# Kernel tuning notes

Measured on AMD Instinct MI355X. Metric: run time of the kernel, lower is better.

The kernel has to match this reference:

```python
import jax, jax.numpy as jnp
import numpy as np

SEGMENT_LENGTHS = [2048, 4096]
DILATION_RATES = [1, 2]


def _group_attention(qg, kg, vg, seg_len, r, gidx):
    # qg/kg/vg: [b, gh, n, d]; segmented dilated attention for one head group.
    b, gh, n, d = qg.shape
    nseg = n // seg_len
    scale = float(1.0 / np.sqrt(d))
    qs = qg.reshape(b, gh, nseg, seg_len, d)
    ks = kg.reshape(b, gh, nseg, seg_len, d)
    vs = vg.reshape(b, gh, nseg, seg_len, d)
    if r > 1:
        m = seg_len // r
        # offset = (group_idx + seg_idx) % r; pattern = offset + r*arange(m) (no wrap since seg_len % r == 0)
        offsets = (gidx + jnp.arange(nseg)) % r            # [nseg]
        idx = offsets[:, None] + r * jnp.arange(m)[None, :]  # [nseg, m]
        si = jnp.arange(nseg)[:, None]                      # [nseg, 1]
        qd = qs[:, :, si, idx]                              # [b, gh, nseg, m, d]
        kd = ks[:, :, si, idx]
        vd = vs[:, :, si, idx]
    else:
        qd, kd, vd = qs, ks, vs
    scores = jnp.einsum('bgsqd,bgskd->bgsqk', qd, kd) * scale
    attn = jax.nn.softmax(scores, axis=-1)
    out = jnp.einsum('bgsqk,bgskd->bgsqd', attn, vd)
    if r > 1:
        # scatter dilated outputs back to their segment positions; unselected positions stay 0
        full = jnp.zeros((b, gh, nseg, seg_len, d), dtype=qg.dtype)
        out = full.at[:, :, si, idx].set(out)
    return out.reshape(b, gh, n, d)


def reference(q, k, v):
    # q, k, v: [b, n, h, d]; ring_size == 1 -> single-device dilated attention
    b, n, h, d = q.shape
    ngroups = len(SEGMENT_LENGTHS)
    gsize = h // ngroups
    qt = jnp.transpose(q, (0, 2, 1, 3))  # [b, h, n, d]
    kt = jnp.transpose(k, (0, 2, 1, 3))
    vt = jnp.transpose(v, (0, 2, 1, 3))
    outs = []
    for i, (s, r) in enumerate(zip(SEGMENT_LENGTHS, DILATION_RATES)):
        hs, he = i * gsize, (i + 1) * gsize
        outs.append(_group_attention(qt[:, hs:he], kt[:, hs:he], vt[:, hs:he], s, r, i))
    out = jnp.concatenate(outs, axis=1)   # [b, h, n, d]
    return jnp.transpose(out, (0, 2, 1, 3))  # [b, n, h, d]


def setup_inputs() -> dict:
    key = jax.random.key(0)
    kq, kk, kv = jax.random.split(key, 3)
    shape = (1, 8192, 16, 128)
    return {
        'q': jax.random.normal(kq, shape, dtype=jnp.float32),
        'k': jax.random.normal(kk, shape, dtype=jnp.float32),
        'v': jax.random.normal(kv, shape, dtype=jnp.float32),
    }
```

## Files before the change

### kernel.cpp

```cpp
#include <hip/hip_runtime.h>
#include <hip/hip_bf16.h>

typedef __attribute__((ext_vector_type(8)))  short bf16x8;
typedef __attribute__((ext_vector_type(4)))  float f32x4;
typedef __attribute__((ext_vector_type(16))) float f32x16;
typedef __attribute__((ext_vector_type(4)))  int   int4v;

__device__ __forceinline__ short f2bf(float f) {
    unsigned u = __builtin_bit_cast(unsigned, f);
    unsigned r = u + 0x7fffu + ((u >> 16) & 1u);
    return (short)(r >> 16);
}

__device__ __forceinline__ int row_map(int p, int j) {
    if (p < 32) return (p & 3) * 2048 + j;
    return ((p - 32) & 1) == 0 ? (2 * j + 1) : (4096 + 2 * j);
}
__device__ __forceinline__ int head_of(int p) {
    return (p < 32) ? (p >> 2) : (8 + ((p - 32) >> 1));
}

__global__ __launch_bounds__(256) void conv_kv_kernel(
    const float* __restrict__ K, const float* __restrict__ V,
    short* __restrict__ Kws, short* __restrict__ Vws)
{
    if (blockIdx.x < 6144) {
        const int cid = blockIdx.x * 256 + threadIdx.x;
        const int p   = cid >> 15;
        const int rem = cid & 32767;
        const int row = rem >> 4;
        const int d8  = (rem & 15) << 3;
        const int g   = row_map(p, row);
        const float* src = K + ((size_t)(g * 16 + head_of(p))) * 128 + d8;
        bf16x8 o;
        #pragma unroll
        for (int e = 0; e < 8; ++e) o[e] = f2bf(src[e]);
        *(bf16x8*)(Kws + (((size_t)p * 2048 + row) << 7) + d8) = o;
        return;
    }
    __shared__ short T[128][72];
    const int b   = blockIdx.x - 6144;
    const int p   = b >> 5;
    const int kb  = b & 31;
    const int tid = threadIdx.x;
    const int h   = head_of(p);
    #pragma unroll
    for (int it = 0; it < 4; ++it) {
        const int cid  = it * 256 + tid;
        const int krow = cid & 63;
        const int d8   = (cid >> 6) << 3;
        const int g = row_map(p, kb * 64 + krow);
        const float* vp = V + ((size_t)(g * 16 + h)) * 128 + d8;
        #pragma unroll
        for (int e = 0; e < 8; ++e) T[d8 + e][krow] = f2bf(vp[e]);
    }
    __syncthreads();
    #pragma unroll
    for (int it = 0; it < 4; ++it) {
        const int j   = it * 256 + tid;
        const int d   = j >> 3;
        const int c16 = j & 7;
        bf16x8 val = *(const bf16x8*)&T[d][c16 * 8];
        *(bf16x8*)(Vws + ((size_t)p * 128 + d) * 2048 + kb * 64 + c16 * 8) = val;
    }
}

__global__ __launch_bounds__(256, 2) void dilated_attn12_kernel(
    const float* __restrict__ Q, const short* __restrict__ Kws,
    const short* __restrict__ Vws, float* __restrict__ O)
{
    __shared__ short Ks[64 * 128];
    __shared__ short Vt[128 * 64];
    __shared__ float sbuf[4][32];

    const int logical = (blockIdx.x & 7) * 96 + (blockIdx.x >> 3);
    const int pid  = logical >> 4;
    const int tile = logical & 15;
    const int h    = head_of(pid);

    const int tid  = threadIdx.x;
    const int wave = tid >> 6;
    const int lane = tid & 63;
    const int ql   = lane & 31;
    const int hi   = lane >> 5;

    const float scale_log2e = 0.08838834764831845f * 1.4426950408889634f;

    const short* Kp = Kws + ((size_t)pid * 2048 << 7);
    const short* Vp = Vws + ((size_t)pid * 128) * 2048;

    bf16x8 qf[8];
    {
        const int j = tile * 128 + wave * 32 + ql;
        const int g = row_map(pid, j);
        const float* qp = Q + ((size_t)(g * 16 + h)) * 128 + hi * 8;
        #pragma unroll
        for (int c = 0; c < 8; ++c) {
            bf16x8 f;
            #pragma unroll
            for (int e = 0; e < 8; ++e) f[e] = f2bf(qp[c * 16 + e] * scale_log2e);
            qf[c] = f;
        }
    }

    f32x16 oacc[4];
    #pragma unroll
    for (int dt = 0; dt < 4; ++dt) oacc[dt] = (f32x16)0.f;
    float l = 0.f;

    const short* kptr[4];
    const short* vptr[4];
    #pragma unroll
    for (int it = 0; it < 4; ++it) {
        const int j = it * 256 + wave * 64 + lane;
        kptr[it] = Kp + (((size_t)(j >> 4)) << 7) + (j & 15) * 8;
        vptr[it] = Vp + ((size_t)(j >> 3)) * 2048 + (j & 7) * 8;
    }
    int4v kreg[4], vreg[4];

    auto LOADR = [&]() {
        #pragma unroll
        for (int it = 0; it < 4; ++it) {
            kreg[it] = *(const int4v*)kptr[it];
            kptr[it] += 64 * 128;
        }
        #pragma unroll
        for (int it = 0; it < 4; ++it) {
            vreg[it] = *(const int4v*)vptr[it];
            vptr[it] += 64;
        }
    };
    auto WRITE = [&]() {
        #pragma unroll
        for (int it = 0; it < 4; ++it) {
            const int j   = it * 256 + wave * 64 + lane;
            const int row = j >> 4;
            const int u   = j & 15;
            *(int4v*)&Ks[row * 128 + ((u ^ (row & 15)) << 3)] = kreg[it];
        }
        #pragma unroll
        for (int it = 0; it < 4; ++it) {
            const int j   = it * 256 + wave * 64 + lane;
            const int row = j >> 3;
            const int u   = j & 7;
            *(int4v*)&Vt[row * 64 + ((u ^ (row & 7)) << 3)] = vreg[it];
        }
    };

    LOADR();
    WRITE();
    __syncthreads();

    for (int t = 0; t < 32; ++t) {
        if (t < 31) LOADR();

        f32x16 p[2];
        __builtin_amdgcn_s_setprio(1);
        #pragma unroll
        for (int kt2 = 0; kt2 < 2; ++kt2) {
            f32x16 acc = (f32x16)(-20.0f);
            const int row = kt2 * 32 + ql;
            #pragma unroll
            for (int c = 0; c < 8; ++c) {
                const int u = 2 * c + hi;
                bf16x8 a = *(const bf16x8*)&Ks[row * 128 + ((u ^ (row & 15)) << 3)];
                acc = __builtin_amdgcn_mfma_f32_32x32x16_bf16(a, qf[c], acc, 0, 0, 0);
            }
            p[kt2] = acc;
        }
        __builtin_amdgcn_s_setprio(0);

        float rs = 0.f;
        #pragma unroll
        for (int kt2 = 0; kt2 < 2; ++kt2)
            #pragma unroll
            for (int r = 0; r < 16; ++r) {
                const float pv = exp2f(p[kt2][r]);
                p[kt2][r] = pv;
                rs += pv;
            }
        l += rs;

        bf16x8 pa[4];
        #pragma unroll
        for (int kt2 = 0; kt2 < 2; ++kt2) {
            int A0, A1, B0, B1, C0, C1, D0, D1;
            asm("v_cvt_pk_bf16_f32 %0,%1,%2" : "=v"(A0) : "v"(p[kt2][0]),  "v"(p[kt2][1]));
            asm("v_cvt_pk_bf16_f32 %0,%1,%2" : "=v"(A1) : "v"(p[kt2][2]),  "v"(p[kt2][3]));
            asm("v_cvt_pk_bf16_f32 %0,%1,%2" : "=v"(B0) : "v"(p[kt2][4]),  "v"(p[kt2][5]));
            asm("v_cvt_pk_bf16_f32 %0,%1,%2" : "=v"(B1) : "v"(p[kt2][6]),  "v"(p[kt2][7]));
            asm("v_cvt_pk_bf16_f32 %0,%1,%2" : "=v"(C0) : "v"(p[kt2][8]),  "v"(p[kt2][9]));
            asm("v_cvt_pk_bf16_f32 %0,%1,%2" : "=v"(C1) : "v"(p[kt2][10]), "v"(p[kt2][11]));
            asm("v_cvt_pk_bf16_f32 %0,%1,%2" : "=v"(D0) : "v"(p[kt2][12]), "v"(p[kt2][13]));
            asm("v_cvt_pk_bf16_f32 %0,%1,%2" : "=v"(D1) : "v"(p[kt2][14]), "v"(p[kt2][15]));
            asm("v_permlane32_swap_b32 %0, %1" : "+v"(A0), "+v"(B0));
            asm("v_permlane32_swap_b32 %0, %1" : "+v"(A1), "+v"(B1));
            asm("v_permlane32_swap_b32 %0, %1" : "+v"(C0), "+v"(D0));
            asm("v_permlane32_swap_b32 %0, %1" : "+v"(C1), "+v"(D1));
            pa[2 * kt2 + 0] = __builtin_bit_cast(bf16x8, (int4v){A0, A1, B0, B1});
            pa[2 * kt2 + 1] = __builtin_bit_cast(bf16x8, (int4v){C0, C1, D0, D1});
        }

        __builtin_amdgcn_s_setprio(1);
        #pragma unroll
        for (int ks = 0; ks < 4; ++ks) {
            #pragma unroll
            for (int dt = 0; dt < 4; ++dt) {
                const int row = dt * 32 + ql;
                const int u   = 2 * ks + hi;
                bf16x8 vb = *(const bf16x8*)&Vt[row * 64 + ((u ^ (row & 7)) << 3)];
                oacc[dt] = __builtin_amdgcn_mfma_f32_32x32x16_bf16(pa[ks], vb, oacc[dt], 0, 0, 0);
            }
        }
        __builtin_amdgcn_s_setprio(0);

        if (t < 31) {
            __syncthreads();
            WRITE();
            __syncthreads();
        }
    }

    l += __shfl_xor(l, 32);
    if (lane < 32) sbuf[wave][lane] = 1.f / l;
    #pragma unroll
    for (int r = 0; r < 16; ++r) {
        const int qrow = (r & 3) + 8 * (r >> 2) + 4 * hi;
        const float inv = sbuf[wave][qrow];
        const int j = tile * 128 + wave * 32 + qrow;
        const int g = row_map(pid, j);
        float* op = O + ((size_t)(g * 16 + h)) * 128 + ql;
        #pragma unroll
        for (int dt = 0; dt < 4; ++dt)
            op[dt * 32] = oacc[dt][r] * inv;
    }
}

__global__ __launch_bounds__(256) void zero_fill_kernel(float* __restrict__ O)
{
    const int t = blockIdx.x * 256 + threadIdx.x;
    const int c4   = t & 31;
    const int rowi = (t >> 5) & 4095;
    const int hh   = t >> 17;
    const int row  = (rowi < 2048) ? (2 * rowi) : (4096 + 2 * (rowi - 2048) + 1);
    float4 z; z.x = 0.f; z.y = 0.f; z.z = 0.f; z.w = 0.f;
    *(float4*)&O[((size_t)(row * 16) + 8 + hh) * 128 + c4 * 4] = z;
}

#define BK    64
#define KPAD  136
#define VPAD  72
__global__ __launch_bounds__(256) void dilated_attn_v1_kernel(
    const float* __restrict__ Q, const float* __restrict__ K,
    const float* __restrict__ V, float* __restrict__ O)
{
    __shared__ short KsL[BK][KPAD];
    __shared__ short VtL[128][VPAD];
    __shared__ short PsL[4][16][VPAD];
    const int bid  = blockIdx.x;
    const int p    = bid >> 5;
    const int tile = bid & 31;
    const int h    = head_of(p);
    const int tid  = threadIdx.x;
    const int wave = tid >> 6;
    const int lane = tid & 63;
    const int lr   = lane & 15;
    const int lg   = lane >> 4;
    const float scale_log2e = 0.08838834764831845f * 1.4426950408889634f;
    bf16x8 qf[4];
    {
        const int j = tile * 64 + wave * 16 + lr;
        const int g = row_map(p, j);
        const float* qp = Q + ((size_t)(g * 16 + h)) * 128 + lg * 8;
        #pragma unroll
        for (int c = 0; c < 4; ++c) {
            bf16x8 f;
            #pragma unroll
            for (int e = 0; e < 8; ++e) f[e] = f2bf(qp[c * 32 + e] * scale_log2e);
            qf[c] = f;
        }
    }
    f32x4 oacc[8];
    #pragma unroll
    for (int i = 0; i < 8; ++i) oacc[i] = (f32x4)0.f;
    float m[4], l[4];
    #pragma unroll
    for (int r = 0; r < 4; ++r) { m[r] = -3.0e38f; l[r] = 0.f; }
    for (int kb = 0; kb < 2048 / BK; ++kb) {
        __syncthreads();
        #pragma unroll
        for (int it = 0; it < 4; ++it) {
            const int cid  = it * 256 + tid;
            const int krow = cid >> 4;
            const int dcol = (cid & 15) << 3;
            const int g = row_map(p, kb * BK + krow);
            const float* kp = K + ((size_t)(g * 16 + h)) * 128 + dcol;
            bf16x8 kk;
            #pragma unroll
            for (int e = 0; e < 8; ++e) kk[e] = f2bf(kp[e]);
            *(bf16x8*)&KsL[krow][dcol] = kk;
        }
        #pragma unroll
        for (int it = 0; it < 4; ++it) {
            const int cid  = it * 256 + tid;
            const int krow = cid & 63;
            const int dcol = (cid >> 6) << 3;
            const int g = row_map(p, kb * BK + krow);
            const float* vp = V + ((size_t)(g * 16 + h)) * 128 + dcol;
            #pragma unroll
            for (int e = 0; e < 8; ++e) VtL[dcol + e][krow] = f2bf(vp[e]);
        }
        __syncthreads();
        f32x4 s[4];
        #pragma unroll
        for (int t = 0; t < 4; ++t) {
            f32x4 acc = (f32x4)0.f;
            #pragma unroll
            for (int c = 0; c < 4; ++c) {
                bf16x8 b = *(const bf16x8*)&KsL[t * 16 + lr][c * 32 + lg * 8];
                acc = __builtin_amdgcn_mfma_f32_16x16x32_bf16(qf[c], b, acc, 0, 0, 0);
            }
            s[t] = acc;
        }
        #pragma unroll
        for (int r = 0; r < 4; ++r) {
            float bm = fmaxf(fmaxf(s[0][r], s[1][r]), fmaxf(s[2][r], s[3][r]));
            bm = fmaxf(bm, __shfl_xor(bm, 1));
            bm = fmaxf(bm, __shfl_xor(bm, 2));
            bm = fmaxf(bm, __shfl_xor(bm, 4));
            bm = fmaxf(bm, __shfl_xor(bm, 8));
            const float mn = fmaxf(m[r], bm);
            const float sf = exp2f(m[r] - mn);
            m[r] = mn;
            float rs = 0.f;
            #pragma unroll
            for (int t = 0; t < 4; ++t) {
                const float pv = exp2f(s[t][r] - mn);
                s[t][r] = pv;
                rs += pv;
            }
            rs += __shfl_xor(rs, 1);
            rs += __shfl_xor(rs, 2);
            rs += __shfl_xor(rs, 4);
            rs += __shfl_xor(rs, 8);
            l[r] = l[r] * sf + rs;
            #pragma unroll
            for (int dt = 0; dt < 8; ++dt) oacc[dt][r] *= sf;
        }
        #pragma unroll
        for (int t = 0; t < 4; ++t)
            #pragma unroll
            for (int r = 0; r < 4; ++r)
                PsL[wave][lg * 4 + r][t * 16 + lr] = f2bf(s[t][r]);
        #pragma unroll
        for (int cc = 0; cc < 2; ++cc) {
            bf16x8 pa = *(const bf16x8*)&PsL[wave][lr][cc * 32 + lg * 8];
            #pragma unroll
            for (int dt = 0; dt < 8; ++dt) {
                bf16x8 vb = *(const bf16x8*)&VtL[dt * 16 + lr][cc * 32 + lg * 8];
                oacc[dt] = __builtin_amdgcn_mfma_f32_16x16x32_bf16(pa, vb, oacc[dt], 0, 0, 0);
            }
        }
    }
    #pragma unroll
    for (int r = 0; r < 4; ++r) {
        const int j = tile * 64 + wave * 16 + lg * 4 + r;
        const int g = row_map(p, j);
        const float inv = 1.f / l[r];
        float* op = O + ((size_t)(g * 16 + h)) * 128 + lr;
        #pragma unroll
        for (int dt = 0; dt < 8; ++dt)
            op[dt * 16] = oacc[dt][r] * inv;
    }
}

extern "C" void kernel_launch(void* const* d_in, const int* in_sizes, int n_in,
                              void* d_out, int out_size, void* d_ws, size_t ws_size,
                              hipStream_t stream) {
    const float* q = (const float*)d_in[0];
    const float* k = (const float*)d_in[1];
    const float* v = (const float*)d_in[2];
    float* o = (float*)d_out;

    const size_t kws_elems = (size_t)48 * 2048 * 128;
    const size_t need = kws_elems * 2 * 2;
    hipLaunchKernelGGL(zero_fill_kernel, dim3(4096), dim3(256), 0, stream, o);
    if (ws_size >= need) {
        short* kws = (short*)d_ws;
        short* vws = kws + kws_elems;
        hipLaunchKernelGGL(conv_kv_kernel, dim3(7680), dim3(256), 0, stream,
                           k, v, kws, vws);
        hipLaunchKernelGGL(dilated_attn12_kernel, dim3(48 * 16), dim3(256), 0, stream,
                           q, kws, vws, o);
    } else {
        hipLaunchKernelGGL(dilated_attn_v1_kernel, dim3(48 * 32), dim3(256), 0, stream,
                           q, k, v, o);
    }
}
```

Measured before the change: 174.6 us.

## Double K/V tile size to 128 keys and interleave QK/PV per 32-key slice

The attention kernel now stages 128 keys of K and V per iteration instead of 64, halving the number of loop iterations and their barrier pairs. Each thread loads 8 contiguous 16-byte chunks per tensor, using a simpler row-per-thread-pair mapping. The inner loop now processes one 32-key slice at a time, running QK, exp and PV back to back, which lowers live score registers. In exchange, shared memory use doubles to about 64 KB per block and register-staged prefetch grows to 16 vectors, which may put the two-blocks-per-CU occupancy target at risk.

Result: slower. 276.4 us (+58.4%).

```diff
diff --git a/kernel.cpp b/kernel.cpp
--- a/kernel.cpp
+++ b/kernel.cpp
@@ -65,12 +65,12 @@
     }
 }
 
-__global__ __launch_bounds__(256, 2) void dilated_attn12_kernel(
+__global__ __launch_bounds__(256, 2) void dilated_attn13_kernel(
     const float* __restrict__ Q, const short* __restrict__ Kws,
     const short* __restrict__ Vws, float* __restrict__ O)
 {
-    __shared__ short Ks[64 * 128];
-    __shared__ short Vt[128 * 64];
+    __shared__ short Ks[128 * 128];
+    __shared__ short Vt[128 * 128];
     __shared__ float sbuf[4][32];
 
     const int logical = (blockIdx.x & 7) * 96 + (blockIdx.x >> 3);
@@ -108,113 +108,98 @@
     for (int dt = 0; dt < 4; ++dt) oacc[dt] = (f32x16)0.f;
     float l = 0.f;
 
-    const short* kptr[4];
-    const short* vptr[4];
-    #pragma unroll
-    for (int it = 0; it < 4; ++it) {
-        const int j = it * 256 + wave * 64 + lane;
-        kptr[it] = Kp + (((size_t)(j >> 4)) << 7) + (j & 15) * 8;
-        vptr[it] = Vp + ((size_t)(j >> 3)) * 2048 + (j & 7) * 8;
-    }
-    int4v kreg[4], vreg[4];
+    const int srow = tid >> 1;
+    const int u0   = (tid & 1) << 3;
+    const int swz  = srow & 15;
+
+    const short* kptr = Kp + (size_t)srow * 128  + u0 * 8;
+    const short* vptr = Vp + (size_t)srow * 2048 + u0 * 8;
+    int4v kreg[8], vreg[8];
 
     auto LOADR = [&]() {
         #pragma unroll
-        for (int it = 0; it < 4; ++it) {
-            kreg[it] = *(const int4v*)kptr[it];
-            kptr[it] += 64 * 128;
-        }
-        #pragma unroll
-        for (int it = 0; it < 4; ++it) {
-            vreg[it] = *(const int4v*)vptr[it];
-            vptr[it] += 64;
-        }
+        for (int it = 0; it < 8; ++it) kreg[it] = *(const int4v*)(kptr + it * 8);
+        #pragma unroll
+        for (int it = 0; it < 8; ++it) vreg[it] = *(const int4v*)(vptr + it * 8);
+        kptr += 128 * 128;
+        vptr += 128;
     };
     auto WRITE = [&]() {
         #pragma unroll
-        for (int it = 0; it < 4; ++it) {
-            const int j   = it * 256 + wave * 64 + lane;
-            const int row = j >> 4;
-            const int u   = j & 15;
-            *(int4v*)&Ks[row * 128 + ((u ^ (row & 15)) << 3)] = kreg[it];
-        }
-        #pragma unroll
-        for (int it = 0; it < 4; ++it) {
-            const int j   = it * 256 + wave * 64 + lane;
-            const int row = j >> 3;
-            const int u   = j & 7;
-            *(int4v*)&Vt[row * 64 + ((u ^ (row & 7)) << 3)] = vreg[it];
-        }
+        for (int it = 0; it < 8; ++it)
+            *(int4v*)&Ks[srow * 128 + (((u0 + it) ^ swz) << 3)] = kreg[it];
+        #pragma unroll
+        for (int it = 0; it < 8; ++it)
+            *(int4v*)&Vt[srow * 128 + (((u0 + it) ^ swz) << 3)] = vreg[it];
     };
 
     LOADR();
     WRITE();
     __syncthreads();
 
-    for (int t = 0; t < 32; ++t) {
-        if (t < 31) LOADR();
-
-        f32x16 p[2];
-        __builtin_amdgcn_s_setprio(1);
-        #pragma unroll
-        for (int kt2 = 0; kt2 < 2; ++kt2) {
-            f32x16 acc = (f32x16)(-20.0f);
-            const int row = kt2 * 32 + ql;
-            #pragma unroll
-            for (int c = 0; c < 8; ++c) {
-                const int u = 2 * c + hi;
-                bf16x8 a = *(const bf16x8*)&Ks[row * 128 + ((u ^ (row & 15)) << 3)];
-                acc = __builtin_amdgcn_mfma_f32_32x32x16_bf16(a, qf[c], acc, 0, 0, 0);
-            }
-            p[kt2] = acc;
-        }
-        __builtin_amdgcn_s_setprio(0);
-
-        float rs = 0.f;
-        #pragma unroll
-        for (int kt2 = 0; kt2 < 2; ++kt2)
+    for (int t = 0; t < 16; ++t) {
+        if (t < 15) LOADR();
+
+        #pragma unroll
+        for (int kt2 = 0; kt2 < 4; ++kt2) {
+            f32x16 p;
+            {
+                f32x16 acc = (f32x16)(-20.0f);
+                const int row = kt2 * 32 + ql;
+                __builtin_amdgcn_s_setprio(1);
+                #pragma unroll
+                for (int c = 0; c < 8; ++c) {
+                    const int u = 2 * c + hi;
+                    bf16x8 a = *(const bf16x8*)&Ks[row * 128 + ((u ^ (row & 15)) << 3)];
+                    acc = __builtin_amdgcn_mfma_f32_32x32x16_bf16(a, qf[c], acc, 0, 0, 0);
+                }
+                __builtin_amdgcn_s_setprio(0);
+                p = acc;
+            }
+
+            float rs = 0.f;
             #pragma unroll
             for (int r = 0; r < 16; ++r) {
-                const float pv = exp2f(p[kt2][r]);
-                p[kt2][r] = pv;
+                const float pv = exp2f(p[r]);
+                p[r] = pv;
                 rs += pv;
             }
-        l += rs;
-
-        bf16x8 pa[4];
-        #pragma unroll
-        for (int kt2 = 0; kt2 < 2; ++kt2) {
-            int A0, A1, B0, B1, C0, C1, D0, D1;
-            asm("v_cvt_pk_bf16_f32 %0,%1,%2" : "=v"(A0) : "v"(p[kt2][0]),  "v"(p[kt2][1]));
-            asm("v_cvt_pk_bf16_f32 %0,%1,%2" : "=v"(A1) : "v"(p[kt2][2]),  "v"(p[kt2][3]));
-            asm("v_cvt_pk_bf16_f32 %0,%1,%2" : "=v"(B0) : "v"(p[kt2][4]),  "v"(p[kt2][5]));
-            asm("v_cvt_pk_bf16_f32 %0,%1,%2" : "=v"(B1) : "v"(p[kt2][6]),  "v"(p[kt2][7]));
-            asm("v_cvt_pk_bf16_f32 %0,%1,%2" : "=v"(C0) : "v"(p[kt2][8]),  "v"(p[kt2][9]));
-            asm("v_cvt_pk_bf16_f32 %0,%1,%2" : "=v"(C1) : "v"(p[kt2][10]), "v"(p[kt2][11]));
-            asm("v_cvt_pk_bf16_f32 %0,%1,%2" : "=v"(D0) : "v"(p[kt2][12]), "v"(p[kt2][13]));
-            asm("v_cvt_pk_bf16_f32 %0,%1,%2" : "=v"(D1) : "v"(p[kt2][14]), "v"(p[kt2][15]));
-            asm("v_permlane32_swap_b32 %0, %1" : "+v"(A0), "+v"(B0));
-            asm("v_permlane32_swap_b32 %0, %1" : "+v"(A1), "+v"(B1));
-            asm("v_permlane32_swap_b32 %0, %1" : "+v"(C0), "+v"(D0));
-            asm("v_permlane32_swap_b32 %0, %1" : "+v"(C1), "+v"(D1));
-            pa[2 * kt2 + 0] = __builtin_bit_cast(bf16x8, (int4v){A0, A1, B0, B1});
-            pa[2 * kt2 + 1] = __builtin_bit_cast(bf16x8, (int4v){C0, C1, D0, D1});
-        }
-
-        __builtin_amdgcn_s_setprio(1);
-        #pragma unroll
-        for (int ks = 0; ks < 4; ++ks) {
-            #pragma unroll
-            for (int dt = 0; dt < 4; ++dt) {
-                const int row = dt * 32 + ql;
-                const int u   = 2 * ks + hi;
-                bf16x8 vb = *(const bf16x8*)&Vt[row * 64 + ((u ^ (row & 7)) << 3)];
-                oacc[dt] = __builtin_amdgcn_mfma_f32_32x32x16_bf16(pa[ks], vb, oacc[dt], 0, 0, 0);
-            }
-        }
-        __builtin_amdgcn_s_setprio(0);
-
-        if (t < 31) {
+            l += rs;
+
+            bf16x8 pa[2];
+            {
+                int A0, A1, B0, B1, C0, C1, D0, D1;
+                asm("v_cvt_pk_bf16_f32 %0,%1,%2" : "=v"(A0) : "v"(p[0]),  "v"(p[1]));
+                asm("v_cvt_pk_bf16_f32 %0,%1,%2" : "=v"(A1) : "v"(p[2]),  "v"(p[3]));
+                asm("v_cvt_pk_bf16_f32 %0,%1,%2" : "=v"(B0) : "v"(p[4]),  "v"(p[5]));
+                asm("v_cvt_pk_bf16_f32 %0,%1,%2" : "=v"(B1) : "v"(p[6]),  "v"(p[7]));
+                asm("v_cvt_pk_bf16_f32 %0,%1,%2" : "=v"(C0) : "v"(p[8]),  "v"(p[9]));
+                asm("v_cvt_pk_bf16_f32 %0,%1,%2" : "=v"(C1) : "v"(p[10]), "v"(p[11]));
+                asm("v_cvt_pk_bf16_f32 %0,%1,%2" : "=v"(D0) : "v"(p[12]), "v"(p[13]));
+                asm("v_cvt_pk_bf16_f32 %0,%1,%2" : "=v"(D1) : "v"(p[14]), "v"(p[15]));
+                asm("v_permlane32_swap_b32 %0, %1" : "+v"(A0), "+v"(B0));
+                asm("v_permlane32_swap_b32 %0, %1" : "+v"(A1), "+v"(B1));
+                asm("v_permlane32_swap_b32 %0, %1" : "+v"(C0), "+v"(D0));
+                asm("v_permlane32_swap_b32 %0, %1" : "+v"(C1), "+v"(D1));
+                pa[0] = __builtin_bit_cast(bf16x8, (int4v){A0, A1, B0, B1});
+                pa[1] = __builtin_bit_cast(bf16x8, (int4v){C0, C1, D0, D1});
+            }
+
+            __builtin_amdgcn_s_setprio(1);
+            #pragma unroll
+            for (int ks2 = 0; ks2 < 2; ++ks2) {
+                const int u = 2 * (kt2 * 2 + ks2) + hi;
+                #pragma unroll
+                for (int dt = 0; dt < 4; ++dt) {
+                    const int row = dt * 32 + ql;
+                    bf16x8 vb = *(const bf16x8*)&Vt[row * 128 + ((u ^ (row & 15)) << 3)];
+                    oacc[dt] = __builtin_amdgcn_mfma_f32_32x32x16_bf16(pa[ks2], vb, oacc[dt], 0, 0, 0);
+                }
+            }
+            __builtin_amdgcn_s_setprio(0);
+        }
+
+        if (t < 15) {
             __syncthreads();
             WRITE();
             __syncthreads();
@@ -390,7 +375,7 @@
         short* vws = kws + kws_elems;
         hipLaunchKernelGGL(conv_kv_kernel, dim3(7680), dim3(256), 0, stream,
                            k, v, kws, vws);
-        hipLaunchKernelGGL(dilated_attn12_kernel, dim3(48 * 16), dim3(256), 0, stream,
+        hipLaunchKernelGGL(dilated_attn13_kernel, dim3(48 * 16), dim3(256), 0, stream,
                            q, kws, vws, o);
     } else {
         hipLaunchKernelGGL(dilated_attn_v1_kernel, dim3(48 * 32), dim3(256), 0, stream,
```
